# Kernel tuning notes

Measured on AMD Instinct MI355X. Metric: run time of the kernel, lower is better.

The kernel has to match this reference:

```python
import jax, jax.numpy as jnp
import numpy as np

GRID = 48
F = GRID * GRID        # number of mesh faces
C = 128                # channels
H = 8                  # attention heads
DH = C // H
B = 2                  # meshes in batch
WID = 256              # SelectionPrediction width


def _bfs_levels():
    """BFS flood-fill levels on a 4-connected GRIDxGRID face graph, anchor at center.
    Returns [n_levels, max_ring] int32, padded with F (dropped on scatter)."""
    c = GRID // 2
    ii, jj = np.meshgrid(np.arange(GRID), np.arange(GRID), indexing='ij')
    d = (np.abs(ii - c) + np.abs(jj - c)).reshape(-1)  # BFS depth == Manhattan dist
    L = int(d.max()) + 1
    Bd = int(np.bincount(d).max())
    idx = np.full((L, Bd), F, dtype=np.int32)
    for lv in range(L):
        faces = np.nonzero(d == lv)[0]
        idx[lv, :faces.size] = faces
    return jnp.asarray(idx)


def setup_inputs() -> dict:
    key = jax.random.key(0)
    ks = jax.random.split(key, 16)
    s = 1.0 / np.sqrt(C)
    sw = 1.0 / np.sqrt(WID)
    return {
        'x':  jax.random.normal(ks[0], (B, C, F), jnp.float32),
        # AnchorAttentionBlock projections (q/k/v/out)
        'Wq': jax.random.normal(ks[1], (C, C), jnp.float32) * s,
        'Wk': jax.random.normal(ks[2], (C, C), jnp.float32) * s,
        'Wv': jax.random.normal(ks[3], (C, C), jnp.float32) * s,
        'Wo': jax.random.normal(ks[4], (C, C), jnp.float32) * s,
        # SelectionPrediction (n_input=C, width=256, depth=3, sigmoid)
        'W1': jax.random.normal(ks[5], (C, WID), jnp.float32) * s,
        'b1': jnp.zeros((WID,), jnp.float32),
        'W2': jax.random.normal(ks[6], (WID, WID), jnp.float32) * sw,
        'b2': jnp.zeros((WID,), jnp.float32),
        'W3': jax.random.normal(ks[7], (WID, WID), jnp.float32) * sw,
        'b3': jnp.zeros((WID,), jnp.float32),
        'W4': jax.random.normal(ks[8], (WID, WID), jnp.float32) * sw,
        'b4': jnp.zeros((WID,), jnp.float32),
        'W5': jax.random.normal(ks[9], (WID, 1), jnp.float32) * sw,
        'b5': jnp.zeros((1,), jnp.float32),
        'levels_idx': _bfs_levels(),
    }


def reference(x, Wq, Wk, Wv, Wo, W1, b1, W2, b2, W3, b3, W4, b4, W5, b5, levels_idx):
    scale = 1.0 / jnp.sqrt(jnp.asarray(DH, x.dtype))

    def flood(feats):                       # feats: [F, C], one mesh
        def step(cur, idx):                 # idx: [Bd] boundary ring (pad = F)
            q = cur[idx]                                    # [Bd, C] (pad rows clamp-gather)
            qh = (q @ Wq).reshape(-1, H, DH)                # [Bd, H, DH]
            kh = (cur @ Wk).reshape(F, H, DH)               # global fftype: keys = all faces
            vh = (cur @ Wv).reshape(F, H, DH)
            att = jax.nn.softmax(jnp.einsum('bhd,fhd->bhf', qh, kh) * scale, axis=-1)
            o = jnp.einsum('bhf,fhd->bhd', att, vh).reshape(-1, C) @ Wo
            new = q + o                                     # mode='resid'
            return cur.at[idx].set(new, mode='drop'), None  # pad idx == F -> dropped
        out, _ = jax.lax.scan(step, feats, levels_idx)
        return out

    final = jax.vmap(flood)(x.transpose(0, 2, 1))           # [B, F, C]
    # SelectionPrediction on final_features.transpose(2,1)
    h = jax.nn.relu(final @ W1 + b1)
    h = jax.nn.relu(h @ W2 + b2)
    h = jax.nn.relu(h @ W3 + b3)
    h = jax.nn.relu(h @ W4 + b4)
    scores = jax.nn.sigmoid(h @ W5 + b5)                    # [B, F, 1] in [0, 1]
    return final.transpose(0, 2, 1), scores
```

## Files before the change

kernel.cpp:

```cpp
#include <hip/hip_runtime.h>
#include <hip/hip_bf16.h>
#include <stdint.h>

#define GRIDN 48
#define F 2304
#define C 128
#define H 8
#define DH 16
#define NB 2
#define WID 256
#define NLV 49
#define SMH (H * 18)
#define LVS 32

typedef __hip_bfloat16 bf16;

__device__ __forceinline__ float b2f(bf16 v) { return __bfloat162float(v); }

__global__ void k_permdetect(const void* __restrict__ x, int* __restrict__ flag,
                             int* __restrict__ permIdx, int* __restrict__ lvflags) {
    __shared__ int cnt[NLV], start[NLV];
    __shared__ int bad;
    int t = threadIdx.x;
    if (t == 0) bad = 0;
    if (t < NLV) cnt[t] = 0;
    for (int i = t; i < NLV * LVS + 32; i += 256) lvflags[i] = 0;
    __syncthreads();
    {
        const bf16* xb = (const bf16*)x;
        int insane = 0;
        #pragma unroll
        for (int i = 0; i < 8; ++i) {
            float v = b2f(xb[t * 8 + i]);
            if (!(fabsf(v) < 1e10f)) insane = 1;
        }
        if (insane) atomicOr(&bad, 1);
    }
    for (int f = t; f < F; f += 256) {
        int d = abs(f / GRIDN - GRIDN / 2) + abs(f % GRIDN - GRIDN / 2);
        atomicAdd(&cnt[d], 1);
    }
    __syncthreads();
    if (t == 0) {
        int s = 0;
        for (int l = 0; l < NLV; ++l) { start[l] = s; s += cnt[l]; }
        *flag = bad;
    }
    __syncthreads();
    for (int f = t; f < F; f += 256) {
        int d = abs(f / GRIDN - GRIDN / 2) + abs(f % GRIDN - GRIDN / 2);
        permIdx[f] = atomicAdd(&start[d], 1);
    }
}

struct WSeg { const void* src; int off; int cnt; };
struct WSegs { WSeg s[14]; };

__global__ void k_convert(WSegs segs, const int* __restrict__ flag,
                          float* __restrict__ dst, int total) {
    int i = blockIdx.x * blockDim.x + threadIdx.x;
    if (i >= total) return;
    bool f32 = (*flag != 0);
    #pragma unroll 1
    for (int j = 0; j < 14; ++j) {
        int off = segs.s[j].off, cnt = segs.s[j].cnt;
        if (i >= off && i < off + cnt) {
            int k = i - off;
            dst[i] = f32 ? ((const float*)segs.s[j].src)[k]
                         : b2f(((const bf16*)segs.s[j].src)[k]);
            return;
        }
    }
}

__global__ void k_wtrans(const float* __restrict__ Wk, const float* __restrict__ Wv,
                         const float* __restrict__ Wo, float* __restrict__ wT) {
    int m = blockIdx.y;
    const float* s = m == 0 ? Wk : (m == 1 ? Wv : Wo);
    int c = blockIdx.x;
    int k = threadIdx.x;
    wT[((size_t)m * C + c) * C + k] = s[k * C + c];
}

__global__ void k_transpose_in(const void* __restrict__ x, const int* __restrict__ flag,
                               float* __restrict__ cur) {
    __shared__ float tile[32][33];
    bool f32 = (*flag != 0);
    int b = blockIdx.z;
    int f0 = blockIdx.x * 32, c0 = blockIdx.y * 32;
    int tx = threadIdx.x, ty = threadIdx.y;
    #pragma unroll
    for (int i = 0; i < 4; ++i) {
        int c = c0 + ty + i * 8;
        size_t idx = ((size_t)b * C + c) * F + f0 + tx;
        tile[ty + i * 8][tx] = f32 ? ((const float*)x)[idx] : b2f(((const bf16*)x)[idx]);
    }
    __syncthreads();
    #pragma unroll
    for (int i = 0; i < 4; ++i) {
        int f = f0 + ty + i * 8;
        cur[((size_t)b * F + f) * C + c0 + tx] = tile[tx][ty + i * 8];
    }
}

__global__ __launch_bounds__(128) void k_proj_init(
        const float* __restrict__ cur, const int* __restrict__ permIdx,
        const float* __restrict__ Wq, const float* __restrict__ Wk, const float* __restrict__ Wv,
        float* __restrict__ qh, float* __restrict__ khT, float* __restrict__ vhT) {
    __shared__ float rows[2][C];
    int r0 = blockIdx.x * 2;
    int tid = threadIdx.x;
    rows[0][tid] = cur[(size_t)r0 * C + tid];
    rows[1][tid] = cur[(size_t)(r0 + 1) * C + tid];
    __syncthreads();
    float aq0 = 0.f, aq1 = 0.f, ak0 = 0.f, ak1 = 0.f, av0 = 0.f, av1 = 0.f;
    for (int k = 0; k < C; ++k) {
        float wq = Wq[k * C + tid];
        float wk = Wk[k * C + tid];
        float wv = Wv[k * C + tid];
        float x0 = rows[0][k], x1 = rows[1][k];
        aq0 = fmaf(x0, wq, aq0); aq1 = fmaf(x1, wq, aq1);
        ak0 = fmaf(x0, wk, ak0); ak1 = fmaf(x1, wk, ak1);
        av0 = fmaf(x0, wv, av0); av1 = fmaf(x1, wv, av1);
    }
    const float scale = 0.25f;
    #pragma unroll
    for (int r = 0; r < 2; ++r) {
        int grow = r0 + r;
        int mesh = grow / F, face = grow % F;
        int p = permIdx[face];
        qh[(size_t)grow * C + tid] = (r == 0 ? aq0 : aq1) * scale;
        khT[((size_t)mesh * C + tid) * F + p] = r == 0 ? ak0 : ak1;
        vhT[((size_t)mesh * C + tid) * F + p] = r == 0 ? av0 : av1;
    }
}

struct Rings { int v[NLV + 1]; };
struct Pairs { int v[NLV + 1]; };

__global__ __launch_bounds__(256) void k_static(
        int Bd, Rings rings, Pairs pairs,
        const int* __restrict__ levels,
        const float* __restrict__ qh_all,
        const float* __restrict__ khT, const float* __restrict__ vhT,
        float* __restrict__ smS) {
    int bx = blockIdx.x;
    int mesh = bx & 1;
    int gp = bx >> 1;
    int lv = 0;
    while (gp >= pairs.v[lv + 1]) ++lv;
    int spair = gp - pairs.v[lv];
    int rs = rings.v[lv];
    int s0 = spair * 2, s1 = s0 + 1;
    int face0 = (s0 < Bd) ? levels[lv * Bd + s0] : F;
    int face1 = (s1 < Bd) ? levels[lv * Bd + s1] : F;
    bool a0 = (face0 >= 0 && face0 < F), a1 = (face1 >= 0 && face1 < F);
    if (!a0 && !a1) return;

    __shared__ float sQh[2][C];
    int tid = threadIdx.x;
    size_t row0 = ((size_t)mesh * F + face0) * C;
    size_t row1 = ((size_t)mesh * F + face1) * C;
    if (tid < C) sQh[0][tid] = a0 ? qh_all[row0 + tid] : 0.f;
    else { int c = tid - C; sQh[1][c] = a1 ? qh_all[row1 + c] : 0.f; }
    __syncthreads();

    int head = tid >> 5, sub = tid & 31;
    float q0[DH], q1[DH];
    #pragma unroll
    for (int d = 0; d < DH; ++d) { q0[d] = sQh[0][head * DH + d]; q1[d] = sQh[1][head * DH + d]; }

    const float* Kb = khT + ((size_t)mesh * C + head * DH) * F;
    const float* Vb = vhT + ((size_t)mesh * C + head * DH) * F;

    float m0 = -1e30f, l0 = 0.f, m1 = -1e30f, l1 = 0.f;
    float acc0[DH], acc1[DH];
    #pragma unroll
    for (int d = 0; d < DH; ++d) { acc0[d] = 0.f; acc1[d] = 0.f; }

    int base0 = rs & ~127;
    for (int base = base0; base < F; base += 128) {
        int p4 = base + 4 * sub;
        float sx0 = 0, sy0 = 0, sz0 = 0, sw0 = 0;
        float sx1 = 0, sy1 = 0, sz1 = 0, sw1 = 0;
        #pragma unroll
        for (int d = 0; d < DH; ++d) {
            float4 kk = *(const float4*)(Kb + d * F + p4);
            float a = q0[d], b = q1[d];
            sx0 = fmaf(a, kk.x, sx0); sy0 = fmaf(a, kk.y, sy0);
            sz0 = fmaf(a, kk.z, sz0); sw0 = fmaf(a, kk.w, sw0);
            sx1 = fmaf(b, kk.x, sx1); sy1 = fmaf(b, kk.y, sy1);
            sz1 = fmaf(b, kk.z, sz1); sw1 = fmaf(b, kk.w, sw1);
        }
        float g0 = 1.f, g1 = 1.f, g2 = 1.f, g3 = 1.f;
        if (base < rs) {
            g0 = (p4     >= rs) ? 1.f : 0.f; g1 = (p4 + 1 >= rs) ? 1.f : 0.f;
            g2 = (p4 + 2 >= rs) ? 1.f : 0.f; g3 = (p4 + 3 >= rs) ? 1.f : 0.f;
        }
        float mx0 = fmaxf(fmaxf(sx0, sy0), fmaxf(sz0, sw0));
        float mn0 = fmaxf(m0, mx0);
        float c0 = __expf(m0 - mn0);
        float px0 = __expf(sx0 - mn0) * g0, py0 = __expf(sy0 - mn0) * g1;
        float pz0 = __expf(sz0 - mn0) * g2, pw0 = __expf(sw0 - mn0) * g3;
        l0 = fmaf(l0, c0, px0 + py0 + pz0 + pw0);
        m0 = mn0;
        float mx1 = fmaxf(fmaxf(sx1, sy1), fmaxf(sz1, sw1));
        float mn1 = fmaxf(m1, mx1);
        float c1e = __expf(m1 - mn1);
        float px1 = __expf(sx1 - mn1) * g0, py1 = __expf(sy1 - mn1) * g1;
        float pz1 = __expf(sz1 - mn1) * g2, pw1 = __expf(sw1 - mn1) * g3;
        l1 = fmaf(l1, c1e, px1 + py1 + pz1 + pw1);
        m1 = mn1;
        #pragma unroll
        for (int d = 0; d < DH; ++d) {
            float4 vv = *(const float4*)(Vb + d * F + p4);
            float w0 = fmaf(px0, vv.x, fmaf(py0, vv.y, fmaf(pz0, vv.z, pw0 * vv.w)));
            float w1 = fmaf(px1, vv.x, fmaf(py1, vv.y, fmaf(pz1, vv.z, pw1 * vv.w)));
            acc0[d] = fmaf(acc0[d], c0, w0);
            acc1[d] = fmaf(acc1[d], c1e, w1);
        }
    }

    #pragma unroll
    for (int w = 16; w >= 1; w >>= 1) {
        float mo = __shfl_xor(m0, w), lo = __shfl_xor(l0, w);
        float mn = fmaxf(m0, mo);
        float ca = __expf(m0 - mn), cb = __expf(mo - mn);
        l0 = l0 * ca + lo * cb;
        #pragma unroll
        for (int d = 0; d < DH; ++d) {
            float ao = __shfl_xor(acc0[d], w);
            acc0[d] = acc0[d] * ca + ao * cb;
        }
        m0 = mn;
        mo = __shfl_xor(m1, w); lo = __shfl_xor(l1, w);
        mn = fmaxf(m1, mo);
        ca = __expf(m1 - mn); cb = __expf(mo - mn);
        l1 = l1 * ca + lo * cb;
        #pragma unroll
        for (int d = 0; d < DH; ++d) {
            float ao = __shfl_xor(acc1[d], w);
            acc1[d] = acc1[d] * ca + ao * cb;
        }
        m1 = mn;
    }
    if (sub == 0) {
        if (a0) {
            float* S = smS + (size_t)(mesh * F + face0) * SMH + head * 18;
            S[0] = m0; S[1] = l0;
            #pragma unroll
            for (int d = 0; d < DH; ++d) S[2 + d] = acc0[d];
        }
        if (a1) {
            float* S = smS + (size_t)(mesh * F + face1) * SMH + head * 18;
            S[0] = m1; S[1] = l1;
            #pragma unroll
            for (int d = 0; d < DH; ++d) S[2 + d] = acc1[d];
        }
    }
}

__global__ __launch_bounds__(256, 4) void k_flood(
        int Bd, Rings rings, Pairs pairs,
        const int* __restrict__ levels, const int* __restrict__ permIdx,
        const float* __restrict__ qh_all, float* __restrict__ cur,
        float* __restrict__ khT, float* __restrict__ vhT,
        const float* __restrict__ smS,
        const float* __restrict__ WkT, const float* __restrict__ WvT,
        const float* __restrict__ WoT,
        int* __restrict__ lvflags, int* __restrict__ lvdone) {
    int bx = blockIdx.x;
    int mesh = bx & 1;
    int gp2 = bx >> 1;
    int lv = 0;
    while (gp2 >= pairs.v[lv + 1]) ++lv;
    int spair = gp2 - pairs.v[lv];

    int s0 = spair * 2, s1 = s0 + 1;
    int face0 = (s0 < Bd) ? levels[lv * Bd + s0] : F;
    int face1 = (s1 < Bd) ? levels[lv * Bd + s1] : F;
    bool a0 = (face0 >= 0 && face0 < F), a1 = (face1 >= 0 && face1 < F);

    __shared__ __attribute__((aligned(16))) float sQh[2][C], sQ[2][C], sRed[2][C], sNew2[2][C];
    __shared__ float sL[2][H];
    __shared__ int sLd;
    int tid = threadIdx.x;
    size_t row0 = ((size_t)mesh * F + face0) * C;
    size_t row1 = ((size_t)mesh * F + face1) * C;
    if (tid < C) {
        if (a0) { sQ[0][tid] = cur[row0 + tid]; sQh[0][tid] = qh_all[row0 + tid]; }
        else    { sQ[0][tid] = 0.f; sQh[0][tid] = 0.f; }
    } else {
        int c = tid - C;
        if (a1) { sQ[1][c] = cur[row1 + c]; sQh[1][c] = qh_all[row1 + c]; }
        else    { sQ[1][c] = 0.f; sQh[1][c] = 0.f; }
    }
    if (tid == 0)
        sLd = __hip_atomic_load(&lvdone[mesh * 16], __ATOMIC_RELAXED, __HIP_MEMORY_SCOPE_AGENT);
    __syncthreads();

    int head = tid >> 5, sub = tid & 31;
    float q0[DH], q1[DH];
    #pragma unroll
    for (int d = 0; d < DH; ++d) { q0[d] = sQh[0][head * DH + d]; q1[d] = sQh[1][head * DH + d]; }

    float* Kb = khT + ((size_t)mesh * C + head * DH) * F;
    float* Vb = vhT + ((size_t)mesh * C + head * DH) * F;

    float m0 = -1e30f, l0 = 0.f, m1 = -1e30f, l1 = 0.f;
    float acc0[DH], acc1[DH];
    #pragma unroll
    for (int d = 0; d < DH; ++d) { acc0[d] = 0.f; acc1[d] = 0.f; }

    #define FOLD_COL(p)                                                                 \
    {                                                                                   \
        float kvv[DH], vv[DH];                                                          \
        _Pragma("unroll")                                                               \
        for (int d = 0; d < DH; ++d)                                                    \
            kvv[d] = __hip_atomic_load(Kb + (size_t)d * F + (p), __ATOMIC_RELAXED,      \
                                       __HIP_MEMORY_SCOPE_AGENT);                       \
        _Pragma("unroll")                                                               \
        for (int d = 0; d < DH; ++d)                                                    \
            vv[d] = __hip_atomic_load(Vb + (size_t)d * F + (p), __ATOMIC_RELAXED,       \
                                      __HIP_MEMORY_SCOPE_AGENT);                        \
        float s0v = 0.f, s1v = 0.f;                                                     \
        _Pragma("unroll")                                                               \
        for (int d = 0; d < DH; ++d) {                                                  \
            s0v = fmaf(q0[d], kvv[d], s0v);                                             \
            s1v = fmaf(q1[d], kvv[d], s1v);                                             \
        }                                                                               \
        float mn0_ = fmaxf(m0, s0v);                                                    \
        float c0_ = __expf(m0 - mn0_), pw0_ = __expf(s0v - mn0_);                       \
        l0 = l0 * c0_ + pw0_;                                                           \
        _Pragma("unroll")                                                               \
        for (int d = 0; d < DH; ++d) acc0[d] = fmaf(acc0[d], c0_, pw0_ * vv[d]);        \
        m0 = mn0_;                                                                      \
        float mn1_ = fmaxf(m1, s1v);                                                    \
        float c1_ = __expf(m1 - mn1_), pw1_ = __expf(s1v - mn1_);                       \
        l1 = l1 * c1_ + pw1_;                                                           \
        _Pragma("unroll")                                                               \
        for (int d = 0; d < DH; ++d) acc1[d] = fmaf(acc1[d], c1_, pw1_ * vv[d]);        \
        m1 = mn1_;                                                                      \
    }

    int ld = sLd;
    if (ld > lv) ld = lv;
    int bulkEnd = rings.v[ld];
    for (int p = sub; p < bulkEnd; p += 32) FOLD_COL(p);

    for (int gpi = ld; gpi < lv; ++gpi) {
        if (tid == 0) {
            int need = pairs.v[gpi + 1] - pairs.v[gpi];
            int* fl = &lvflags[gpi * LVS + mesh * 16];
            int guard = 0;
            while (__hip_atomic_load(fl, __ATOMIC_RELAXED, __HIP_MEMORY_SCOPE_AGENT) < need
                   && guard < (1 << 22)) {
                __builtin_amdgcn_s_sleep(2);
                ++guard;
            }
        }
        __syncthreads();
        int frs = rings.v[gpi], fre = rings.v[gpi + 1];
        for (int p = frs + sub; p < fre; p += 32) FOLD_COL(p);
    }
    #undef FOLD_COL

    #pragma unroll
    for (int w = 16; w >= 1; w >>= 1) {
        float mo = __shfl_xor(m0, w), lo = __shfl_xor(l0, w);
        float mn = fmaxf(m0, mo);
        float ca = __expf(m0 - mn), cb = __expf(mo - mn);
        l0 = l0 * ca + lo * cb;
        #pragma unroll
        for (int d = 0; d < DH; ++d) {
            float ao = __shfl_xor(acc0[d], w);
            acc0[d] = acc0[d] * ca + ao * cb;
        }
        m0 = mn;
        mo = __shfl_xor(m1, w); lo = __shfl_xor(l1, w);
        mn = fmaxf(m1, mo);
        ca = __expf(m1 - mn); cb = __expf(mo - mn);
        l1 = l1 * ca + lo * cb;
        #pragma unroll
        for (int d = 0; d < DH; ++d) {
            float ao = __shfl_xor(acc1[d], w);
            acc1[d] = acc1[d] * ca + ao * cb;
        }
        m1 = mn;
    }
    if (sub == 0) {
        {
            int fr = a0 ? face0 : 0;
            const float* S = smS + (size_t)(mesh * F + fr) * SMH + head * 18;
            float ms = S[0], ls = S[1];
            float mn = fmaxf(m0, ms);
            float ca = __expf(m0 - mn), cb = __expf(ms - mn);
            sL[0][head] = l0 * ca + ls * cb;
            #pragma unroll
            for (int d = 0; d < DH; ++d)
                sRed[0][head * DH + d] = fmaf(acc0[d], ca, S[2 + d] * cb);
        }
        {
            int fr = a1 ? face1 : 0;
            const float* S = smS + (size_t)(mesh * F + fr) * SMH + head * 18;
            float ms = S[0], ls = S[1];
            float mn = fmaxf(m1, ms);
            float ca = __expf(m1 - mn), cb = __expf(ms - mn);
            sL[1][head] = l1 * ca + ls * cb;
            #pragma unroll
            for (int d = 0; d < DH; ++d)
                sRed[1][head * DH + d] = fmaf(acc1[d], ca, S[2 + d] * cb);
        }
    }
    __syncthreads();
    if (tid < C) sRed[0][tid] = sRed[0][tid] / sL[0][tid >> 4];
    else { int c = tid - C; sRed[1][c] = sRed[1][c] / sL[1][c >> 4]; }
    __syncthreads();

    {
        int j = tid >> 7;
        int c = tid & 127;
        bool act = j == 0 ? a0 : a1;
        float o = 0.f;
        const float4* WoR = (const float4*)(WoT + (size_t)c * C);
        const float4* Rr  = (const float4*)(&sRed[j][0]);
        #pragma unroll
        for (int k4 = 0; k4 < C / 4; ++k4) {
            float4 w = WoR[k4];
            float4 r = Rr[k4];
            o = fmaf(r.x, w.x, o); o = fmaf(r.y, w.y, o);
            o = fmaf(r.z, w.z, o); o = fmaf(r.w, w.w, o);
        }
        float nv = sQ[j][c] + o;
        sNew2[j][c] = nv;
        if (act) cur[(j == 0 ? row0 : row1) + c] = nv;
    }
    __syncthreads();

    if (lv != NLV - 1) {
        int j = tid >> 7;
        bool act = j == 0 ? a0 : a1;
        if (act) {
            int facej = j == 0 ? face0 : face1;
            int p = permIdx[facej];
            int isV = (tid >> 6) & 1;
            int c2 = (tid & 63) * 2;
            const float* WT = isV ? WvT : WkT;
            float aa = 0.f, ab = 0.f;
            const float4* Wa = (const float4*)(WT + (size_t)c2 * C);
            const float4* Wb = (const float4*)(WT + (size_t)(c2 + 1) * C);
            const float4* Nr = (const float4*)(&sNew2[j][0]);
            #pragma unroll
            for (int k4 = 0; k4 < C / 4; ++k4) {
                float4 x = Nr[k4];
                float4 wa = Wa[k4], wb = Wb[k4];
                aa = fmaf(x.x, wa.x, aa); aa = fmaf(x.y, wa.y, aa);
                aa = fmaf(x.z, wa.z, aa); aa = fmaf(x.w, wa.w, aa);
                ab = fmaf(x.x, wb.x, ab); ab = fmaf(x.y, wb.y, ab);
                ab = fmaf(x.z, wb.z, ab); ab = fmaf(x.w, wb.w, ab);
            }
            float* B = (isV ? vhT : khT) + (size_t)mesh * C * F + p;
            __hip_atomic_store(B + (size_t)c2 * F, aa,
                               __ATOMIC_RELAXED, __HIP_MEMORY_SCOPE_AGENT);
            __hip_atomic_store(B + (size_t)(c2 + 1) * F, ab,
                               __ATOMIC_RELAXED, __HIP_MEMORY_SCOPE_AGENT);
        }
        __syncthreads();
        if (tid == 0) {
            int need = pairs.v[lv + 1] - pairs.v[lv];
            int old = __hip_atomic_fetch_add(&lvflags[lv * LVS + mesh * 16], 1,
                                             __ATOMIC_RELAXED, __HIP_MEMORY_SCOPE_AGENT);
            if (old == need - 1)
                __hip_atomic_fetch_max(&lvdone[mesh * 16], lv + 1,
                                       __ATOMIC_RELAXED, __HIP_MEMORY_SCOPE_AGENT);
        }
    }
}

__global__ __launch_bounds__(256) void k_mlp(
        const float* __restrict__ cur,
        const float* __restrict__ W1, const float* __restrict__ b1,
        const float* __restrict__ W2, const float* __restrict__ b2,
        const float* __restrict__ W3, const float* __restrict__ b3,
        const float* __restrict__ W4, const float* __restrict__ b4,
        const float* __restrict__ W5, const float* __restrict__ b5,
        float* __restrict__ out_scores) {
    __shared__ float sIn[2][C];
    __shared__ float sA[2][WID];
    __shared__ float sB[2][WID];
    int tid = threadIdx.x;
    int r0 = blockIdx.x * 2;
    for (int i = tid; i < 2 * C; i += 256) sIn[i >> 7][i & 127] = cur[(size_t)r0 * C + i];
    __syncthreads();
    {
        float a0 = 0.f, a1 = 0.f;
        for (int k = 0; k < C; ++k) {
            float w = W1[k * WID + tid];
            a0 = fmaf(sIn[0][k], w, a0);
            a1 = fmaf(sIn[1][k], w, a1);
        }
        float bias = b1[tid];
        sA[0][tid] = fmaxf(a0 + bias, 0.f);
        sA[1][tid] = fmaxf(a1 + bias, 0.f);
    }
    __syncthreads();
    {
        float a0 = 0.f, a1 = 0.f;
        for (int k = 0; k < WID; ++k) {
            float w = W2[k * WID + tid];
            a0 = fmaf(sA[0][k], w, a0);
            a1 = fmaf(sA[1][k], w, a1);
        }
        float bias = b2[tid];
        sB[0][tid] = fmaxf(a0 + bias, 0.f);
        sB[1][tid] = fmaxf(a1 + bias, 0.f);
    }
    __syncthreads();
    {
        float a0 = 0.f, a1 = 0.f;
        for (int k = 0; k < WID; ++k) {
            float w = W3[k * WID + tid];
            a0 = fmaf(sB[0][k], w, a0);
            a1 = fmaf(sB[1][k], w, a1);
        }
        float bias = b3[tid];
        sA[0][tid] = fmaxf(a0 + bias, 0.f);
        sA[1][tid] = fmaxf(a1 + bias, 0.f);
    }
    __syncthreads();
    {
        float a0 = 0.f, a1 = 0.f;
        for (int k = 0; k < WID; ++k) {
            float w = W4[k * WID + tid];
            a0 = fmaf(sA[0][k], w, a0);
            a1 = fmaf(sA[1][k], w, a1);
        }
        float bias = b4[tid];
        sB[0][tid] = fmaxf(a0 + bias, 0.f);
        sB[1][tid] = fmaxf(a1 + bias, 0.f);
    }
    __syncthreads();
    if (tid < 2) {
        float a = b5[0];
        for (int k = 0; k < WID; ++k) a = fmaf(sB[tid][k], W5[k], a);
        out_scores[r0 + tid] = 1.f / (1.f + __expf(-a));
    }
}

__global__ void k_transpose_out(const float* __restrict__ cur, float* __restrict__ out) {
    __shared__ float tile[32][33];
    int b = blockIdx.z;
    int f0 = blockIdx.x * 32, c0 = blockIdx.y * 32;
    int tx = threadIdx.x, ty = threadIdx.y;
    #pragma unroll
    for (int i = 0; i < 4; ++i) {
        int f = f0 + ty + i * 8;
        tile[ty + i * 8][tx] = cur[((size_t)b * F + f) * C + c0 + tx];
    }
    __syncthreads();
    #pragma unroll
    for (int i = 0; i < 4; ++i) {
        int c = c0 + ty + i * 8;
        out[((size_t)b * C + c) * F + f0 + tx] = tile[tx][ty + i * 8];
    }
}

extern "C" void kernel_launch(void* const* d_in, const int* in_sizes, int n_in,
                              void* d_out, int out_size, void* d_ws, size_t ws_size,
                              hipStream_t stream) {
    const int* levels = (const int*)d_in[15];
    int Bd = in_sizes[15] / NLV;

    const size_t n = (size_t)NB * F * C;
    float* cur  = (float*)d_ws;
    float* qh   = cur + n;
    float* khT  = qh + n;
    float* vhT  = khT + n;
    float* wbuf = vhT + n;
    float* wT   = wbuf + 296196;
    int*   permIdx = (int*)(wT + 49152);
    int*   flag = permIdx + F;
    int*   lvflags = permIdx + 2320;
    int*   lvdone = lvflags + NLV * LVS;
    float* smS  = (float*)(permIdx + 4096);

    const int oWq = 0,       oWk = 16384,  oWv = 32768,  oWo = 49152;
    const int oW1 = 65536,   oB1 = 98304;
    const int oW2 = 98560,   oB2 = 164096;
    const int oW3 = 164352,  oB3 = 229888;
    const int oW4 = 230144,  oB4 = 295680;
    const int oW5 = 295936,  oB5 = 296192;
    const int wtot = 296193;

    WSegs segs = {{
        { d_in[1],  oWq, 16384 }, { d_in[2],  oWk, 16384 },
        { d_in[3],  oWv, 16384 }, { d_in[4],  oWo, 16384 },
        { d_in[5],  oW1, 32768 }, { d_in[6],  oB1, 256 },
        { d_in[7],  oW2, 65536 }, { d_in[8],  oB2, 256 },
        { d_in[9],  oW3, 65536 }, { d_in[10], oB3, 256 },
        { d_in[11], oW4, 65536 }, { d_in[12], oB4, 256 },
        { d_in[13], oW5, 256 },   { d_in[14], oB5, 1 },
    }};

    Rings rings;
    Pairs pairs;
    int totPairs = 0;
    {
        int cnt[NLV];
        for (int l = 0; l < NLV; ++l) cnt[l] = 0;
        for (int i = 0; i < GRIDN; ++i)
            for (int j = 0; j < GRIDN; ++j)
                cnt[(i < 24 ? 24 - i : i - 24) + (j < 24 ? 24 - j : j - 24)]++;
        rings.v[0] = 0;
        pairs.v[0] = 0;
        for (int l = 0; l < NLV; ++l) {
            rings.v[l + 1] = rings.v[l] + cnt[l];
            pairs.v[l + 1] = pairs.v[l] + (cnt[l] + 1) / 2;
        }
        totPairs = pairs.v[NLV];
    }

    float* out0 = (float*)d_out;
    float* out1 = out0 + (size_t)NB * C * F;

    k_permdetect<<<1, 256, 0, stream>>>(d_in[0], flag, permIdx, lvflags);
    k_convert<<<(wtot + 255) / 256, 256, 0, stream>>>(segs, flag, wbuf, wtot);
    k_wtrans<<<dim3(C, 3), C, 0, stream>>>(wbuf + oWk, wbuf + oWv, wbuf + oWo, wT);
    k_transpose_in<<<dim3(F / 32, C / 32, NB), dim3(32, 8), 0, stream>>>(d_in[0], flag, cur);
    k_proj_init<<<(NB * F) / 2, 128, 0, stream>>>(cur, permIdx, wbuf + oWq, wbuf + oWk, wbuf + oWv,
                                                  qh, khT, vhT);

    k_static<<<2 * totPairs, 256, 0, stream>>>(Bd, rings, pairs, levels, qh, khT, vhT, smS);

    k_flood<<<2 * totPairs, 256, 0, stream>>>(Bd, rings, pairs, levels, permIdx, qh, cur,
                                              khT, vhT, smS,
                                              wT, wT + 16384, wT + 32768,
                                              lvflags, lvdone);

    k_mlp<<<(NB * F) / 2, 256, 0, stream>>>(cur, wbuf + oW1, wbuf + oB1, wbuf + oW2, wbuf + oB2,
                                            wbuf + oW3, wbuf + oB3, wbuf + oW4, wbuf + oB4,
                                            wbuf + oW5, wbuf + oB5, out1);
    k_transpose_out<<<dim3(F / 32, C / 32, NB), dim3(32, 8), 0, stream>>>(cur, out0);
}
```

Measured before the change: 1.272 ms.

## Vectorize attention fold over 4 keys per lane and tier spin-wait sleeps

Adds a fast path to the online-softmax fold in which each lane loads float4 chunks of K and V and processes four consecutive key columns at once. It does one max/rescale per four keys instead of one per key, which cuts the exp and rescale work and improves memory coalescing. Unaligned edges fall back to the old per-column fold. It also makes the spin-wait sleep length depend on how far the awaited level is from the current one, which reduces polling traffic on distant levels but may add latency.

```diff
diff --git a/kernel.cpp b/kernel.cpp
--- a/kernel.cpp
+++ b/kernel.cpp
@@ -343,27 +343,80 @@
         m1 = mn1_;                                                                      \
     }
 
+    #define FOLD_FAST(LO, HI)                                                           \
+    for (int base = (LO) & ~127; base < (HI); base += 128) {                            \
+        int p4 = base + 4 * sub;                                                        \
+        if (p4 >= (LO) && p4 + 4 <= (HI)) {                                             \
+            float sx0 = 0, sy0 = 0, sz0 = 0, sw0 = 0;                                   \
+            float sx1 = 0, sy1 = 0, sz1 = 0, sw1 = 0;                                   \
+            _Pragma("unroll")                                                           \
+            for (int d = 0; d < DH; ++d) {                                              \
+                float4 kk = *(const float4*)(Kb + (size_t)d * F + p4);                  \
+                float a = q0[d], b = q1[d];                                             \
+                sx0 = fmaf(a, kk.x, sx0); sy0 = fmaf(a, kk.y, sy0);                     \
+                sz0 = fmaf(a, kk.z, sz0); sw0 = fmaf(a, kk.w, sw0);                     \
+                sx1 = fmaf(b, kk.x, sx1); sy1 = fmaf(b, kk.y, sy1);                     \
+                sz1 = fmaf(b, kk.z, sz1); sw1 = fmaf(b, kk.w, sw1);                     \
+            }                                                                           \
+            float mx0 = fmaxf(fmaxf(sx0, sy0), fmaxf(sz0, sw0));                        \
+            float mn0 = fmaxf(m0, mx0);                                                 \
+            float c0 = __expf(m0 - mn0);                                                \
+            float px0 = __expf(sx0 - mn0), py0 = __expf(sy0 - mn0);                     \
+            float pz0 = __expf(sz0 - mn0), pw0 = __expf(sw0 - mn0);                     \
+            l0 = fmaf(l0, c0, px0 + py0 + pz0 + pw0);                                   \
+            m0 = mn0;                                                                   \
+            float mx1 = fmaxf(fmaxf(sx1, sy1), fmaxf(sz1, sw1));                        \
+            float mn1 = fmaxf(m1, mx1);                                                 \
+            float c1e = __expf(m1 - mn1);                                               \
+            float px1 = __expf(sx1 - mn1), py1 = __expf(sy1 - mn1);                     \
+            float pz1 = __expf(sz1 - mn1), pw1 = __expf(sw1 - mn1);                     \
+            l1 = fmaf(l1, c1e, px1 + py1 + pz1 + pw1);                                  \
+            m1 = mn1;                                                                   \
+            _Pragma("unroll")                                                           \
+            for (int d = 0; d < DH; ++d) {                                              \
+                float4 vv = *(const float4*)(Vb + (size_t)d * F + p4);                  \
+                float w0 = fmaf(px0, vv.x, fmaf(py0, vv.y, fmaf(pz0, vv.z, pw0 * vv.w))); \
+                float w1 = fmaf(px1, vv.x, fmaf(py1, vv.y, fmaf(pz1, vv.z, pw1 * vv.w))); \
+                acc0[d] = fmaf(acc0[d], c0, w0);                                        \
+                acc1[d] = fmaf(acc1[d], c1e, w1);                                       \
+            }                                                                           \
+        }                                                                               \
+    }
+
     int ld = sLd;
     if (ld > lv) ld = lv;
     int bulkEnd = rings.v[ld];
-    for (int p = sub; p < bulkEnd; p += 32) FOLD_COL(p);
+    int bFast = bulkEnd & ~15;
+    FOLD_FAST(0, bFast);
+    for (int p = bFast + sub; p < bulkEnd; p += 32) FOLD_COL(p);
 
     for (int gpi = ld; gpi < lv; ++gpi) {
         if (tid == 0) {
             int need = pairs.v[gpi + 1] - pairs.v[gpi];
             int* fl = &lvflags[gpi * LVS + mesh * 16];
+            int dist = lv - 1 - gpi;
             int guard = 0;
             while (__hip_atomic_load(fl, __ATOMIC_RELAXED, __HIP_MEMORY_SCOPE_AGENT) < need
                    && guard < (1 << 22)) {
-                __builtin_amdgcn_s_sleep(2);
+                if (dist == 0) __builtin_amdgcn_s_sleep(1);
+                else if (dist < 4) __builtin_amdgcn_s_sleep(16);
+                else __builtin_amdgcn_s_sleep(64);
                 ++guard;
             }
         }
         __syncthreads();
         int frs = rings.v[gpi], fre = rings.v[gpi + 1];
-        for (int p = frs + sub; p < fre; p += 32) FOLD_COL(p);
+        int aLo = (frs + 15) & ~15, aHi = fre & ~15;
+        if (aLo < aHi) {
+            for (int p = frs + sub; p < aLo; p += 32) FOLD_COL(p);
+            FOLD_FAST(aLo, aHi);
+            for (int p = aHi + sub; p < fre; p += 32) FOLD_COL(p);
+        } else {
+            for (int p = frs + sub; p < fre; p += 32) FOLD_COL(p);
+        }
     }
     #undef FOLD_COL
+    #undef FOLD_FAST
 
     #pragma unroll
     for (int w = 16; w >= 1; w >>= 1) {
```

Measured after the change: 1.549 ms. 21.8% more time.

## Split flood kernel into seven-level phase launches with dynamic partial-softmax accumulation

Applied to the files above, without the earlier changes.

Replaces the single persistent flood kernel, which relied on cross-block spin-waiting per level, with a sequence of phase kernels that each cover a group of seven levels. Blocks for levels beyond the current group fold the previous group's finished rings into a per-face dynamic online-softmax accumulator (dynS) with vectorized float4 loads. Only the in-group chain still waits on level flags. This aims to cut spin-wait latency and use launch boundaries for coarse synchronization. The cost is seven launches, extra dynS read-modify-write traffic and a larger workspace.

```diff
diff --git a/kernel.cpp b/kernel.cpp
--- a/kernel.cpp
+++ b/kernel.cpp
@@ -12,6 +12,7 @@
 #define NLV 49
 #define SMH (H * 18)
 #define LVS 32
+#define GLV 7
 
 typedef __hip_bfloat16 bf16;
 
@@ -143,7 +144,7 @@
         const int* __restrict__ levels,
         const float* __restrict__ qh_all,
         const float* __restrict__ khT, const float* __restrict__ vhT,
-        float* __restrict__ smS) {
+        float* __restrict__ smS, float* __restrict__ dynS) {
     int bx = blockIdx.x;
     int mesh = bx & 1;
     int gp = bx >> 1;
@@ -247,43 +248,51 @@
     if (sub == 0) {
         if (a0) {
             float* S = smS + (size_t)(mesh * F + face0) * SMH + head * 18;
+            float* D = dynS + (size_t)(mesh * F + face0) * SMH + head * 18;
             S[0] = m0; S[1] = l0;
+            D[0] = -1e30f; D[1] = 0.f;
             #pragma unroll
-            for (int d = 0; d < DH; ++d) S[2 + d] = acc0[d];
+            for (int d = 0; d < DH; ++d) { S[2 + d] = acc0[d]; D[2 + d] = 0.f; }
         }
         if (a1) {
             float* S = smS + (size_t)(mesh * F + face1) * SMH + head * 18;
+            float* D = dynS + (size_t)(mesh * F + face1) * SMH + head * 18;
             S[0] = m1; S[1] = l1;
+            D[0] = -1e30f; D[1] = 0.f;
             #pragma unroll
-            for (int d = 0; d < DH; ++d) S[2 + d] = acc1[d];
-        }
-    }
-}
-
-__global__ __launch_bounds__(256, 4) void k_flood(
-        int Bd, Rings rings, Pairs pairs,
+            for (int d = 0; d < DH; ++d) { S[2 + d] = acc1[d]; D[2 + d] = 0.f; }
+        }
+    }
+}
+
+__global__ __launch_bounds__(256, 4) void k_phase(
+        int g, int Bd, Rings rings, Pairs pairs,
         const int* __restrict__ levels, const int* __restrict__ permIdx,
         const float* __restrict__ qh_all, float* __restrict__ cur,
         float* __restrict__ khT, float* __restrict__ vhT,
-        const float* __restrict__ smS,
+        const float* __restrict__ smS, float* __restrict__ dynS,
         const float* __restrict__ WkT, const float* __restrict__ WvT,
         const float* __restrict__ WoT,
-        int* __restrict__ lvflags, int* __restrict__ lvdone) {
+        int* __restrict__ lvflags) {
     int bx = blockIdx.x;
     int mesh = bx & 1;
-    int gp2 = bx >> 1;
-    int lv = 0;
+    int gp2 = pairs.v[GLV * g] + (bx >> 1);
+    int lv = GLV * g;
     while (gp2 >= pairs.v[lv + 1]) ++lv;
+    bool isChain = (lv < GLV * g + GLV);
+    int rsA = (g == 0) ? 0 : rings.v[GLV * (g - 1)];
+    int rsB = rings.v[GLV * g];
+    if (!isChain && rsA == rsB) return;
+
     int spair = gp2 - pairs.v[lv];
-
     int s0 = spair * 2, s1 = s0 + 1;
     int face0 = (s0 < Bd) ? levels[lv * Bd + s0] : F;
     int face1 = (s1 < Bd) ? levels[lv * Bd + s1] : F;
     bool a0 = (face0 >= 0 && face0 < F), a1 = (face1 >= 0 && face1 < F);
+    if (!isChain && !a0 && !a1) return;
 
     __shared__ __attribute__((aligned(16))) float sQh[2][C], sQ[2][C], sRed[2][C], sNew2[2][C];
     __shared__ float sL[2][H];
-    __shared__ int sLd;
     int tid = threadIdx.x;
     size_t row0 = ((size_t)mesh * F + face0) * C;
     size_t row1 = ((size_t)mesh * F + face1) * C;
@@ -295,8 +304,6 @@
         if (a1) { sQ[1][c] = cur[row1 + c]; sQh[1][c] = qh_all[row1 + c]; }
         else    { sQ[1][c] = 0.f; sQh[1][c] = 0.f; }
     }
-    if (tid == 0)
-        sLd = __hip_atomic_load(&lvdone[mesh * 16], __ATOMIC_RELAXED, __HIP_MEMORY_SCOPE_AGENT);
     __syncthreads();
 
     int head = tid >> 5, sub = tid & 31;
@@ -312,58 +319,94 @@
     #pragma unroll
     for (int d = 0; d < DH; ++d) { acc0[d] = 0.f; acc1[d] = 0.f; }
 
-    #define FOLD_COL(p)                                                                 \
-    {                                                                                   \
-        float kvv[DH], vv[DH];                                                          \
-        _Pragma("unroll")                                                               \
-        for (int d = 0; d < DH; ++d)                                                    \
-            kvv[d] = __hip_atomic_load(Kb + (size_t)d * F + (p), __ATOMIC_RELAXED,      \
-                                       __HIP_MEMORY_SCOPE_AGENT);                       \
-        _Pragma("unroll")                                                               \
-        for (int d = 0; d < DH; ++d)                                                    \
-            vv[d] = __hip_atomic_load(Vb + (size_t)d * F + (p), __ATOMIC_RELAXED,       \
-                                      __HIP_MEMORY_SCOPE_AGENT);                        \
-        float s0v = 0.f, s1v = 0.f;                                                     \
-        _Pragma("unroll")                                                               \
-        for (int d = 0; d < DH; ++d) {                                                  \
-            s0v = fmaf(q0[d], kvv[d], s0v);                                             \
-            s1v = fmaf(q1[d], kvv[d], s1v);                                             \
-        }                                                                               \
-        float mn0_ = fmaxf(m0, s0v);                                                    \
-        float c0_ = __expf(m0 - mn0_), pw0_ = __expf(s0v - mn0_);                       \
-        l0 = l0 * c0_ + pw0_;                                                           \
-        _Pragma("unroll")                                                               \
-        for (int d = 0; d < DH; ++d) acc0[d] = fmaf(acc0[d], c0_, pw0_ * vv[d]);        \
-        m0 = mn0_;                                                                      \
-        float mn1_ = fmaxf(m1, s1v);                                                    \
-        float c1_ = __expf(m1 - mn1_), pw1_ = __expf(s1v - mn1_);                       \
-        l1 = l1 * c1_ + pw1_;                                                           \
-        _Pragma("unroll")                                                               \
-        for (int d = 0; d < DH; ++d) acc1[d] = fmaf(acc1[d], c1_, pw1_ * vv[d]);        \
-        m1 = mn1_;                                                                      \
-    }
-
-    int ld = sLd;
-    if (ld > lv) ld = lv;
-    int bulkEnd = rings.v[ld];
-    for (int p = sub; p < bulkEnd; p += 32) FOLD_COL(p);
-
-    for (int gpi = ld; gpi < lv; ++gpi) {
-        if (tid == 0) {
-            int need = pairs.v[gpi + 1] - pairs.v[gpi];
-            int* fl = &lvflags[gpi * LVS + mesh * 16];
-            int guard = 0;
-            while (__hip_atomic_load(fl, __ATOMIC_RELAXED, __HIP_MEMORY_SCOPE_AGENT) < need
-                   && guard < (1 << 22)) {
-                __builtin_amdgcn_s_sleep(2);
-                ++guard;
+    for (int base = rsA & ~127; base < rsB; base += 128) {
+        int p4 = base + 4 * sub;
+        float sx0 = 0, sy0 = 0, sz0 = 0, sw0 = 0;
+        float sx1 = 0, sy1 = 0, sz1 = 0, sw1 = 0;
+        #pragma unroll
+        for (int d = 0; d < DH; ++d) {
+            float4 kk = *(const float4*)(Kb + (size_t)d * F + p4);
+            float a = q0[d], b = q1[d];
+            sx0 = fmaf(a, kk.x, sx0); sy0 = fmaf(a, kk.y, sy0);
+            sz0 = fmaf(a, kk.z, sz0); sw0 = fmaf(a, kk.w, sw0);
+            sx1 = fmaf(b, kk.x, sx1); sy1 = fmaf(b, kk.y, sy1);
+            sz1 = fmaf(b, kk.z, sz1); sw1 = fmaf(b, kk.w, sw1);
+        }
+        float g0 = (p4     >= rsA && p4     < rsB) ? 1.f : 0.f;
+        float g1 = (p4 + 1 >= rsA && p4 + 1 < rsB) ? 1.f : 0.f;
+        float g2 = (p4 + 2 >= rsA && p4 + 2 < rsB) ? 1.f : 0.f;
+        float g3 = (p4 + 3 >= rsA && p4 + 3 < rsB) ? 1.f : 0.f;
+        float mx0 = fmaxf(fmaxf(sx0, sy0), fmaxf(sz0, sw0));
+        float mn0 = fmaxf(m0, mx0);
+        float c0 = __expf(m0 - mn0);
+        float px0 = __expf(sx0 - mn0) * g0, py0 = __expf(sy0 - mn0) * g1;
+        float pz0 = __expf(sz0 - mn0) * g2, pw0 = __expf(sw0 - mn0) * g3;
+        l0 = fmaf(l0, c0, px0 + py0 + pz0 + pw0);
+        m0 = mn0;
+        float mx1 = fmaxf(fmaxf(sx1, sy1), fmaxf(sz1, sw1));
+        float mn1 = fmaxf(m1, mx1);
+        float c1e = __expf(m1 - mn1);
+        float px1 = __expf(sx1 - mn1) * g0, py1 = __expf(sy1 - mn1) * g1;
+        float pz1 = __expf(sz1 - mn1) * g2, pw1 = __expf(sw1 - mn1) * g3;
+        l1 = fmaf(l1, c1e, px1 + py1 + pz1 + pw1);
+        m1 = mn1;
+        #pragma unroll
+        for (int d = 0; d < DH; ++d) {
+            float4 vv = *(const float4*)(Vb + (size_t)d * F + p4);
+            float w0 = fmaf(px0, vv.x, fmaf(py0, vv.y, fmaf(pz0, vv.z, pw0 * vv.w)));
+            float w1 = fmaf(px1, vv.x, fmaf(py1, vv.y, fmaf(pz1, vv.z, pw1 * vv.w)));
+            acc0[d] = fmaf(acc0[d], c0, w0);
+            acc1[d] = fmaf(acc1[d], c1e, w1);
+        }
+    }
+
+    if (isChain) {
+        for (int gpi = GLV * g; gpi < lv; ++gpi) {
+            if (tid == 0) {
+                int need = pairs.v[gpi + 1] - pairs.v[gpi];
+                int* fl = &lvflags[gpi * LVS + mesh * 16];
+                int dist = lv - 1 - gpi;
+                int guard = 0;
+                while (__hip_atomic_load(fl, __ATOMIC_RELAXED, __HIP_MEMORY_SCOPE_AGENT) < need
+                       && guard < (1 << 22)) {
+                    if (dist == 0) __builtin_amdgcn_s_sleep(1);
+                    else __builtin_amdgcn_s_sleep(16);
+                    ++guard;
+                }
             }
-        }
-        __syncthreads();
-        int frs = rings.v[gpi], fre = rings.v[gpi + 1];
-        for (int p = frs + sub; p < fre; p += 32) FOLD_COL(p);
-    }
-    #undef FOLD_COL
+            __syncthreads();
+            int frs = rings.v[gpi], fre = rings.v[gpi + 1];
+            for (int p = frs + sub; p < fre; p += 32) {
+                float kvv[DH], vv[DH];
+                #pragma unroll
+                for (int d = 0; d < DH; ++d)
+                    kvv[d] = __hip_atomic_load(Kb + (size_t)d * F + p, __ATOMIC_RELAXED,
+                                               __HIP_MEMORY_SCOPE_AGENT);
+                #pragma unroll
+                for (int d = 0; d < DH; ++d)
+                    vv[d] = __hip_atomic_load(Vb + (size_t)d * F + p, __ATOMIC_RELAXED,
+                                              __HIP_MEMORY_SCOPE_AGENT);
+                float s0v = 0.f, s1v = 0.f;
+                #pragma unroll
+                for (int d = 0; d < DH; ++d) {
+                    s0v = fmaf(q0[d], kvv[d], s0v);
+                    s1v = fmaf(q1[d], kvv[d], s1v);
+                }
+                float mn0 = fmaxf(m0, s0v);
+                float c0 = __expf(m0 - mn0), pw0 = __expf(s0v - mn0);
+                l0 = l0 * c0 + pw0;
+                #pragma unroll
+                for (int d = 0; d < DH; ++d) acc0[d] = fmaf(acc0[d], c0, pw0 * vv[d]);
+                m0 = mn0;
+                float mn1 = fmaxf(m1, s1v);
+                float c1 = __expf(m1 - mn1), pw1 = __expf(s1v - mn1);
+                l1 = l1 * c1 + pw1;
+                #pragma unroll
+                for (int d = 0; d < DH; ++d) acc1[d] = fmaf(acc1[d], c1, pw1 * vv[d]);
+                m1 = mn1;
+            }
+        }
+    }
 
     #pragma unroll
     for (int w = 16; w >= 1; w >>= 1) {
@@ -388,13 +431,46 @@
         }
         m1 = mn;
     }
+
+    if (!isChain) {
+        if (sub == 0) {
+            if (a0) {
+                float* D = dynS + (size_t)(mesh * F + face0) * SMH + head * 18;
+                float md = D[0], ldv = D[1];
+                float mn = fmaxf(m0, md);
+                float ca = __expf(m0 - mn), cb = __expf(md - mn);
+                D[0] = mn; D[1] = l0 * ca + ldv * cb;
+                #pragma unroll
+                for (int d = 0; d < DH; ++d) D[2 + d] = fmaf(acc0[d], ca, D[2 + d] * cb);
+            }
+            if (a1) {
+                float* D = dynS + (size_t)(mesh * F + face1) * SMH + head * 18;
+                float md = D[0], ldv = D[1];
+                float mn = fmaxf(m1, md);
+                float ca = __expf(m1 - mn), cb = __expf(md - mn);
+                D[0] = mn; D[1] = l1 * ca + ldv * cb;
+                #pragma unroll
+                for (int d = 0; d < DH; ++d) D[2 + d] = fmaf(acc1[d], ca, D[2 + d] * cb);
+            }
+        }
+        return;
+    }
+
     if (sub == 0) {
         {
             int fr = a0 ? face0 : 0;
+            const float* D = dynS + (size_t)(mesh * F + fr) * SMH + head * 18;
+            float md = D[0], ldv = D[1];
+            float mn = fmaxf(m0, md);
+            float ca = __expf(m0 - mn), cb = __expf(md - mn);
+            l0 = l0 * ca + ldv * cb;
+            #pragma unroll
+            for (int d = 0; d < DH; ++d) acc0[d] = fmaf(acc0[d], ca, D[2 + d] * cb);
+            m0 = mn;
             const float* S = smS + (size_t)(mesh * F + fr) * SMH + head * 18;
             float ms = S[0], ls = S[1];
-            float mn = fmaxf(m0, ms);
-            float ca = __expf(m0 - mn), cb = __expf(ms - mn);
+            mn = fmaxf(m0, ms);
+            ca = __expf(m0 - mn); cb = __expf(ms - mn);
             sL[0][head] = l0 * ca + ls * cb;
             #pragma unroll
             for (int d = 0; d < DH; ++d)
@@ -402,10 +478,18 @@
         }
         {
             int fr = a1 ? face1 : 0;
+            const float* D = dynS + (size_t)(mesh * F + fr) * SMH + head * 18;
+            float md = D[0], ldv = D[1];
+            float mn = fmaxf(m1, md);
+            float ca = __expf(m1 - mn), cb = __expf(md - mn);
+            l1 = l1 * ca + ldv * cb;
+            #pragma unroll
+            for (int d = 0; d < DH; ++d) acc1[d] = fmaf(acc1[d], ca, D[2 + d] * cb);
+            m1 = mn;
             const float* S = smS + (size_t)(mesh * F + fr) * SMH + head * 18;
             float ms = S[0], ls = S[1];
-            float mn = fmaxf(m1, ms);
-            float ca = __expf(m1 - mn), cb = __expf(ms - mn);
+            mn = fmaxf(m1, ms);
+            ca = __expf(m1 - mn); cb = __expf(ms - mn);
             sL[1][head] = l1 * ca + ls * cb;
             #pragma unroll
             for (int d = 0; d < DH; ++d)
@@ -467,12 +551,8 @@
         }
         __syncthreads();
         if (tid == 0) {
-            int need = pairs.v[lv + 1] - pairs.v[lv];
-            int old = __hip_atomic_fetch_add(&lvflags[lv * LVS + mesh * 16], 1,
-                                             __ATOMIC_RELAXED, __HIP_MEMORY_SCOPE_AGENT);
-            if (old == need - 1)
-                __hip_atomic_fetch_max(&lvdone[mesh * 16], lv + 1,
-                                       __ATOMIC_RELAXED, __HIP_MEMORY_SCOPE_AGENT);
+            __hip_atomic_fetch_add(&lvflags[lv * LVS + mesh * 16], 1,
+                                   __ATOMIC_RELAXED, __HIP_MEMORY_SCOPE_AGENT);
         }
     }
 }
@@ -581,8 +661,8 @@
     int*   permIdx = (int*)(wT + 49152);
     int*   flag = permIdx + F;
     int*   lvflags = permIdx + 2320;
-    int*   lvdone = lvflags + NLV * LVS;
     float* smS  = (float*)(permIdx + 4096);
+    float* dynS = smS + (size_t)NB * F * SMH;
 
     const int oWq = 0,       oWk = 16384,  oWv = 32768,  oWo = 49152;
     const int oW1 = 65536,   oB1 = 98304;
@@ -630,12 +710,15 @@
     k_proj_init<<<(NB * F) / 2, 128, 0, stream>>>(cur, permIdx, wbuf + oWq, wbuf + oWk, wbuf + oWv,
                                                   qh, khT, vhT);
 
-    k_static<<<2 * totPairs, 256, 0, stream>>>(Bd, rings, pairs, levels, qh, khT, vhT, smS);
-
-    k_flood<<<2 * totPairs, 256, 0, stream>>>(Bd, rings, pairs, levels, permIdx, qh, cur,
-                                              khT, vhT, smS,
-                                              wT, wT + 16384, wT + 32768,
-                                              lvflags, lvdone);
+    k_static<<<2 * totPairs, 256, 0, stream>>>(Bd, rings, pairs, levels, qh, khT, vhT, smS, dynS);
+
+    for (int g = 0; g < NLV / GLV; ++g) {
+        int gpBase = pairs.v[GLV * g];
+        int nblk = 2 * (totPairs - gpBase);
+        k_phase<<<nblk, 256, 0, stream>>>(g, Bd, rings, pairs, levels, permIdx, qh, cur,
+                                          khT, vhT, smS, dynS,
+                                          wT, wT + 16384, wT + 32768, lvflags);
+    }
 
     k_mlp<<<(NB * F) / 2, 256, 0, stream>>>(cur, wbuf + oW1, wbuf + oB1, wbuf + oW2, wbuf + oB2,
                                             wbuf + oW3, wbuf + oB3, wbuf + oW4, wbuf + oB4,
```

New measurement: 1.348 ms. +6.0%, slower.
